# Kernel tuning notes

Hardware: AMD Instinct MI355X
Metric: run time of the kernel (lower is better)

Reference implementation:

```python
import jax, jax.numpy as jnp
import numpy as np

B, N, F = 16384, 2048, 64

def setup_inputs() -> dict:
    key = jax.random.key(0)
    k1, k2, k3, k4 = jax.random.split(key, 4)
    x = jax.random.normal(k1, (B, N), dtype=jnp.float32)
    # params ~ uniform(-0.1, 0.1) as in torch init
    w0 = jax.random.uniform(k2, (1,), dtype=jnp.float32, minval=-0.1, maxval=0.1)
    w1 = jax.random.uniform(k3, (N,), dtype=jnp.float32, minval=-0.1, maxval=0.1)
    v = jax.random.uniform(k4, (N, F), dtype=jnp.float32, minval=-0.1, maxval=0.1)
    return {"x": x, "w0": w0, "w1": w1, "v": v}

def reference(x, w0, w1, v):
    # FM identity: out_b = w0 + x_b . w1 + 0.5 * sum_f ((x_b . v_:f)^2 - (x_b^2 . v_:f^2))
    linear = x @ w1                                  # [B]
    xv = x @ v                                       # [B, F]
    x2v2 = (x * x) @ (v * v)                         # [B, F]
    pairwise = 0.5 * jnp.sum(xv * xv - x2v2, axis=-1)  # [B]
    return w0[0] + linear + pairwise
```

## Files before the change

### kernel.cpp

```cpp
#include <hip/hip_runtime.h>

#define N_DIM 2048
#define F_DIM 64

typedef __attribute__((ext_vector_type(4))) float  f32x4;
typedef __attribute__((ext_vector_type(8))) short  s16x8;
typedef __attribute__((ext_vector_type(8))) __bf16 bf16x8;

static __device__ __forceinline__ unsigned short f2bf(float f) {
  unsigned int u = __builtin_bit_cast(unsigned int, f);
  u += 0x7fffu + ((u >> 16) & 1u);
  return (unsigned short)(u >> 16);
}

__global__ __launch_bounds__(256) void fm_prep(const float* __restrict__ v,
                                               unsigned short* __restrict__ vb,
                                               float* __restrict__ sh) {
  const int blk = blockIdx.x;
  const int tid = threadIdx.x;
  if (blk < 64) {
    const int g  = blk * 256 + tid;
    const int fl = g & 63;
    const int t  = (g >> 6) & 3;
    const int kt = g >> 8;
    const int kbase = kt * 32 + ((fl >> 4) << 3);
    const int f = t * 16 + (fl & 15);
    s16x8 a;
#pragma unroll
    for (int j = 0; j < 8; ++j)
      a[j] = (short)f2bf(v[(size_t)(kbase + j) * F_DIM + f]);
    *(s16x8*)(vb + (size_t)g * 8) = a;
  } else {
    const int k = (blk - 64) * 256 + tid;
    const f32x4* row = (const f32x4*)(v + (size_t)k * F_DIM);
    float s = 0.0f;
#pragma unroll
    for (int i = 0; i < 16; ++i) {
      f32x4 q = row[i];
      s += q[0]*q[0] + q[1]*q[1] + q[2]*q[2] + q[3]*q[3];
    }
    sh[k] = 0.5f * s;
  }
}

__global__ __launch_bounds__(256) void fm_main(const float* __restrict__ x,
                                               const float* __restrict__ w0,
                                               const float* __restrict__ w1,
                                               const unsigned short* __restrict__ vb,
                                               const float* __restrict__ sh,
                                               float* __restrict__ out) {
  const int tid  = threadIdx.x;
  const int lane = tid & 63;
  const int w    = tid >> 6;
  const int rowbase = blockIdx.x * 16;
  const int lrow = lane & 15;
  const int ksub = (lane >> 4) << 3;

  __shared__ float w1L[N_DIM];
  __shared__ float shL[N_DIM];
  __shared__ f32x4 accLDS[3][4][64];
  __shared__ float linLDS[4][16];

  const int kw = w * 512;
  const float* xrow = x + (size_t)(rowbase + lrow) * N_DIM + kw;
  const unsigned short* vbase = vb + ((size_t)(w * 64) * 64 + lane) * 8;

  f32x4 pxa[2], pxb[2];
  s16x8 pb[2][4];
  pxa[0] = *(const f32x4*)(xrow + ksub);
  pxb[0] = *(const f32x4*)(xrow + ksub + 4);
#pragma unroll
  for (int t = 0; t < 4; ++t)
    pb[0][t] = *(const s16x8*)(vbase + t * 512);

  {
    const int t8 = tid * 8;
    *(f32x4*)(&w1L[t8])     = *(const f32x4*)(w1 + t8);
    *(f32x4*)(&w1L[t8 + 4]) = *(const f32x4*)(w1 + t8 + 4);
    *(f32x4*)(&shL[t8])     = *(const f32x4*)(sh + t8);
    *(f32x4*)(&shL[t8 + 4]) = *(const f32x4*)(sh + t8 + 4);
  }
  __syncthreads();

  const float* w1q = w1L + kw;
  const float* shq = shL + kw;

  f32x4 accv[4] = {};
  float lin = 0.0f;

#pragma unroll
  for (int s = 0; s < 16; ++s) {
    const int cur = s & 1, nxt = cur ^ 1;
    if (s < 15) {
      const int kc = (s + 1) * 32 + ksub;
      pxa[nxt] = *(const f32x4*)(xrow + kc);
      pxb[nxt] = *(const f32x4*)(xrow + kc + 4);
      const unsigned short* vbp = vbase + (size_t)(s + 1) * 2048;
#pragma unroll
      for (int t = 0; t < 4; ++t)
        pb[nxt][t] = *(const s16x8*)(vbp + t * 512);
    }
    const int kc = s * 32 + ksub;
    f32x4 wa = *(const f32x4*)(w1q + kc);
    f32x4 wb = *(const f32x4*)(w1q + kc + 4);
    f32x4 sa = *(const f32x4*)(shq + kc);
    f32x4 sb = *(const f32x4*)(shq + kc + 4);
    f32x4 xa = pxa[cur], xb = pxb[cur];
    bf16x8 A;
#pragma unroll
    for (int i = 0; i < 4; ++i) {
      lin = fmaf(xa[i], wa[i] - xa[i] * sa[i], lin);
      lin = fmaf(xb[i], wb[i] - xb[i] * sb[i], lin);
      A[i]     = (__bf16)xa[i];
      A[4 + i] = (__bf16)xb[i];
    }
#pragma unroll
    for (int t = 0; t < 4; ++t)
      accv[t] = __builtin_amdgcn_mfma_f32_16x16x32_bf16(
          A, __builtin_bit_cast(bf16x8, pb[cur][t]), accv[t], 0, 0, 0);
  }

  lin += __shfl_xor(lin, 16);
  lin += __shfl_xor(lin, 32);

  if (w > 0) {
#pragma unroll
    for (int t = 0; t < 4; ++t)
      accLDS[w - 1][t][lane] = accv[t];
  }
  if (lane < 16) linLDS[w][lane] = lin;
  __syncthreads();

  if (w == 0) {
#pragma unroll
    for (int ww = 0; ww < 3; ++ww)
#pragma unroll
      for (int t = 0; t < 4; ++t)
        accv[t] += accLDS[ww][t][lane];

    float p[4];
#pragma unroll
    for (int r = 0; r < 4; ++r) {
      p[r] = 0.0f;
#pragma unroll
      for (int t = 0; t < 4; ++t)
        p[r] += accv[t][r] * accv[t][r];
      p[r] += __shfl_xor(p[r], 1);
      p[r] += __shfl_xor(p[r], 2);
      p[r] += __shfl_xor(p[r], 4);
      p[r] += __shfl_xor(p[r], 8);
    }
    if ((lane & 15) == 0) {
      const int g = lane >> 4;
      const float w0v = w0[0];
#pragma unroll
      for (int r = 0; r < 4; ++r) {
        const int row = g * 4 + r;
        float lt = linLDS[0][row] + linLDS[1][row] + linLDS[2][row] + linLDS[3][row];
        out[rowbase + row] = w0v + lt + 0.5f * p[r];
      }
    }
  }
}

extern "C" void kernel_launch(void* const* d_in, const int* in_sizes, int n_in,
                              void* d_out, int out_size, void* d_ws, size_t ws_size,
                              hipStream_t stream) {
  const float* x  = (const float*)d_in[0];
  const float* w0 = (const float*)d_in[1];
  const float* w1 = (const float*)d_in[2];
  const float* v  = (const float*)d_in[3];
  float* out = (float*)d_out;

  unsigned short* vb = (unsigned short*)d_ws;
  float* sh = (float*)(vb + 131072);

  fm_prep<<<72, 256, 0, stream>>>(v, vb, sh);
  fm_main<<<1024, 256, 0, stream>>>(x, w0, w1, vb, sh, out);
}
```

Measured before the change: 35.43 us.

## Process 32 rows per block with 8 waves splitting K, reusing V fragments

Each block now handles 32 rows instead of 16 using 512 threads. Each of 8 waves covers a 256-wide K slice and issues two MFMAs per loaded V fragment, so V traffic per row is halved. Partial accumulators are combined through a two-stage tree reduction in LDS. This raises register use and adds extra barriers, and the grid drops to 512 blocks.

```diff
diff --git a/kernel.cpp b/kernel.cpp
--- a/kernel.cpp
+++ b/kernel.cpp
@@ -43,122 +43,165 @@
   }
 }
 
-__global__ __launch_bounds__(256) void fm_main(const float* __restrict__ x,
-                                               const float* __restrict__ w0,
-                                               const float* __restrict__ w1,
-                                               const unsigned short* __restrict__ vb,
-                                               const float* __restrict__ sh,
-                                               float* __restrict__ out) {
+__global__ __launch_bounds__(512, 4) void fm_main(const float* __restrict__ x,
+                                                  const float* __restrict__ w0,
+                                                  const float* __restrict__ w1,
+                                                  const unsigned short* __restrict__ vb,
+                                                  const float* __restrict__ sh,
+                                                  float* __restrict__ out) {
   const int tid  = threadIdx.x;
   const int lane = tid & 63;
   const int w    = tid >> 6;
-  const int rowbase = blockIdx.x * 16;
-  const int lrow = lane & 15;
-  const int ksub = (lane >> 4) << 3;
-
-  __shared__ float w1L[N_DIM];
-  __shared__ float shL[N_DIM];
-  __shared__ f32x4 accLDS[3][4][64];
-  __shared__ float linLDS[4][16];
-
-  const int kw = w * 512;
-  const float* xrow = x + (size_t)(rowbase + lrow) * N_DIM + kw;
-  const unsigned short* vbase = vb + ((size_t)(w * 64) * 64 + lane) * 8;
-
-  f32x4 pxa[2], pxb[2];
+  const int rowbase = blockIdx.x * 32;
+  const int g8   = ((lane >> 4) << 3);
+
+  __shared__ __align__(16) float w1L[N_DIM];
+  __shared__ __align__(16) float shL[N_DIM];
+  __shared__ __align__(16) f32x4 accW[4][8][64];
+  __shared__ float linL[8][2][16];
+
+  const int kw = w * 256;
+  const float* xA = x + (size_t)(rowbase + (lane & 15)) * N_DIM + kw + g8;
+  const float* xB = xA + 16 * N_DIM;
+  const unsigned short* vbase = vb + ((size_t)w * 2048 + lane) * 8;
+
+  f32x4 pxa[2], pxb[2], pxc[2], pxd[2];
   s16x8 pb[2][4];
-  pxa[0] = *(const f32x4*)(xrow + ksub);
-  pxb[0] = *(const f32x4*)(xrow + ksub + 4);
+  pxa[0] = *(const f32x4*)(xA);
+  pxb[0] = *(const f32x4*)(xA + 4);
+  pxc[0] = *(const f32x4*)(xB);
+  pxd[0] = *(const f32x4*)(xB + 4);
 #pragma unroll
   for (int t = 0; t < 4; ++t)
     pb[0][t] = *(const s16x8*)(vbase + t * 512);
 
   {
-    const int t8 = tid * 8;
-    *(f32x4*)(&w1L[t8])     = *(const f32x4*)(w1 + t8);
-    *(f32x4*)(&w1L[t8 + 4]) = *(const f32x4*)(w1 + t8 + 4);
-    *(f32x4*)(&shL[t8])     = *(const f32x4*)(sh + t8);
-    *(f32x4*)(&shL[t8 + 4]) = *(const f32x4*)(sh + t8 + 4);
-  }
-  __syncthreads();
-
-  const float* w1q = w1L + kw;
-  const float* shq = shL + kw;
-
-  f32x4 accv[4] = {};
-  float lin = 0.0f;
-
-#pragma unroll
-  for (int s = 0; s < 16; ++s) {
+    const int t4 = tid << 2;
+    *(f32x4*)&w1L[t4] = *(const f32x4*)(w1 + t4);
+    *(f32x4*)&shL[t4] = *(const f32x4*)(sh + t4);
+  }
+  __syncthreads();
+
+  f32x4 acc[2][4] = {};
+  float linA = 0.0f, linB = 0.0f;
+
+#pragma unroll
+  for (int s = 0; s < 8; ++s) {
     const int cur = s & 1, nxt = cur ^ 1;
-    if (s < 15) {
-      const int kc = (s + 1) * 32 + ksub;
-      pxa[nxt] = *(const f32x4*)(xrow + kc);
-      pxb[nxt] = *(const f32x4*)(xrow + kc + 4);
-      const unsigned short* vbp = vbase + (size_t)(s + 1) * 2048;
+    if (s < 7) {
+      const int kc = (s + 1) * 32;
+      pxa[nxt] = *(const f32x4*)(xA + kc);
+      pxb[nxt] = *(const f32x4*)(xA + kc + 4);
+      pxc[nxt] = *(const f32x4*)(xB + kc);
+      pxd[nxt] = *(const f32x4*)(xB + kc + 4);
+      const unsigned short* vbp = vbase + (s + 1) * 2048;
 #pragma unroll
       for (int t = 0; t < 4; ++t)
         pb[nxt][t] = *(const s16x8*)(vbp + t * 512);
     }
-    const int kc = s * 32 + ksub;
-    f32x4 wa = *(const f32x4*)(w1q + kc);
-    f32x4 wb = *(const f32x4*)(w1q + kc + 4);
-    f32x4 sa = *(const f32x4*)(shq + kc);
-    f32x4 sb = *(const f32x4*)(shq + kc + 4);
-    f32x4 xa = pxa[cur], xb = pxb[cur];
-    bf16x8 A;
+    const int ki = kw + s * 32 + g8;
+    f32x4 xa = pxa[cur], xb = pxb[cur], xc = pxc[cur], xd = pxd[cur];
+    {
+      f32x4 wa = *(const f32x4*)(&w1L[ki]);
+      f32x4 wbv = *(const f32x4*)(&w1L[ki + 4]);
+      f32x4 sa = *(const f32x4*)(&shL[ki]);
+      f32x4 sb = *(const f32x4*)(&shL[ki + 4]);
+#pragma unroll
+      for (int i = 0; i < 4; ++i) {
+        linA = fmaf(xa[i], wa[i]  - xa[i] * sa[i], linA);
+        linA = fmaf(xb[i], wbv[i] - xb[i] * sb[i], linA);
+        linB = fmaf(xc[i], wa[i]  - xc[i] * sa[i], linB);
+        linB = fmaf(xd[i], wbv[i] - xd[i] * sb[i], linB);
+      }
+    }
+    bf16x8 Alo, Ahi;
 #pragma unroll
     for (int i = 0; i < 4; ++i) {
-      lin = fmaf(xa[i], wa[i] - xa[i] * sa[i], lin);
-      lin = fmaf(xb[i], wb[i] - xb[i] * sb[i], lin);
-      A[i]     = (__bf16)xa[i];
-      A[4 + i] = (__bf16)xb[i];
-    }
-#pragma unroll
-    for (int t = 0; t < 4; ++t)
-      accv[t] = __builtin_amdgcn_mfma_f32_16x16x32_bf16(
-          A, __builtin_bit_cast(bf16x8, pb[cur][t]), accv[t], 0, 0, 0);
-  }
-
-  lin += __shfl_xor(lin, 16);
-  lin += __shfl_xor(lin, 32);
-
-  if (w > 0) {
-#pragma unroll
-    for (int t = 0; t < 4; ++t)
-      accLDS[w - 1][t][lane] = accv[t];
-  }
-  if (lane < 16) linLDS[w][lane] = lin;
+      Alo[i]     = (__bf16)xa[i];
+      Alo[4 + i] = (__bf16)xb[i];
+      Ahi[i]     = (__bf16)xc[i];
+      Ahi[4 + i] = (__bf16)xd[i];
+    }
+#pragma unroll
+    for (int t = 0; t < 4; ++t) {
+      bf16x8 Bv = __builtin_bit_cast(bf16x8, pb[cur][t]);
+      acc[0][t] = __builtin_amdgcn_mfma_f32_16x16x32_bf16(Alo, Bv, acc[0][t], 0, 0, 0);
+      acc[1][t] = __builtin_amdgcn_mfma_f32_16x16x32_bf16(Ahi, Bv, acc[1][t], 0, 0, 0);
+    }
+  }
+
+  linA += __shfl_xor(linA, 16);
+  linA += __shfl_xor(linA, 32);
+  linB += __shfl_xor(linB, 16);
+  linB += __shfl_xor(linB, 32);
+  if (lane < 16) {
+    linL[w][0][lane] = linA;
+    linL[w][1][lane] = linB;
+  }
+
+  if (w >= 4) {
+#pragma unroll
+    for (int h = 0; h < 2; ++h)
+#pragma unroll
+      for (int t = 0; t < 4; ++t)
+        accW[w - 4][h * 4 + t][lane] = acc[h][t];
+  }
+  __syncthreads();
+  if (w < 4) {
+#pragma unroll
+    for (int h = 0; h < 2; ++h)
+#pragma unroll
+      for (int t = 0; t < 4; ++t)
+        acc[h][t] += accW[w][h * 4 + t][lane];
+  }
+  __syncthreads();
+  if (w >= 1 && w < 4) {
+#pragma unroll
+    for (int h = 0; h < 2; ++h)
+#pragma unroll
+      for (int t = 0; t < 4; ++t)
+        accW[w - 1][h * 4 + t][lane] = acc[h][t];
+  }
   __syncthreads();
 
   if (w == 0) {
 #pragma unroll
     for (int ww = 0; ww < 3; ++ww)
 #pragma unroll
-      for (int t = 0; t < 4; ++t)
-        accv[t] += accLDS[ww][t][lane];
-
-    float p[4];
-#pragma unroll
-    for (int r = 0; r < 4; ++r) {
-      p[r] = 0.0f;
-#pragma unroll
-      for (int t = 0; t < 4; ++t)
-        p[r] += accv[t][r] * accv[t][r];
-      p[r] += __shfl_xor(p[r], 1);
-      p[r] += __shfl_xor(p[r], 2);
-      p[r] += __shfl_xor(p[r], 4);
-      p[r] += __shfl_xor(p[r], 8);
-    }
+      for (int h = 0; h < 2; ++h)
+#pragma unroll
+        for (int t = 0; t < 4; ++t)
+          acc[h][t] += accW[ww][h * 4 + t][lane];
+
+    float p[2][4];
+#pragma unroll
+    for (int h = 0; h < 2; ++h)
+#pragma unroll
+      for (int r = 0; r < 4; ++r) {
+        float q = 0.0f;
+#pragma unroll
+        for (int t = 0; t < 4; ++t)
+          q += acc[h][t][r] * acc[h][t][r];
+        q += __shfl_xor(q, 1);
+        q += __shfl_xor(q, 2);
+        q += __shfl_xor(q, 4);
+        q += __shfl_xor(q, 8);
+        p[h][r] = q;
+      }
     if ((lane & 15) == 0) {
       const int g = lane >> 4;
       const float w0v = w0[0];
 #pragma unroll
-      for (int r = 0; r < 4; ++r) {
-        const int row = g * 4 + r;
-        float lt = linLDS[0][row] + linLDS[1][row] + linLDS[2][row] + linLDS[3][row];
-        out[rowbase + row] = w0v + lt + 0.5f * p[r];
-      }
+      for (int h = 0; h < 2; ++h)
+#pragma unroll
+        for (int r = 0; r < 4; ++r) {
+          const int row = g * 4 + r;
+          float lt = 0.0f;
+#pragma unroll
+          for (int ww = 0; ww < 8; ++ww)
+            lt += linL[ww][h][row];
+          out[rowbase + h * 16 + row] = w0v + lt + 0.5f * p[h][r];
+        }
     }
   }
 }
@@ -176,5 +219,5 @@
   float* sh = (float*)(vb + 131072);
 
   fm_prep<<<72, 256, 0, stream>>>(v, vb, sh);
-  fm_main<<<1024, 256, 0, stream>>>(x, w0, w1, vb, sh, out);
-}
+  fm_main<<<512, 512, 0, stream>>>(x, w0, w1, vb, sh, out);
+}
```

Result: slower. 45.13 us (+27.4%).
